# Performance work log

Measured on AMD Instinct MI355X. Metric: run time of the kernel, lower is better.

Reference implementation:

```python
import jax, jax.numpy as jnp
import numpy as np

ANNEAL_T_START = 5.0
T_END = 1.0


def setup_inputs() -> dict:
    key = jax.random.key(0)
    ks = jax.random.split(key, 8)
    B, V, H, CD, WID = 8192, 1024, 128, 16, 64
    return {
        "cond": jax.random.normal(ks[0], (B, CD), jnp.float32),
        "W": 0.01 * jax.random.normal(ks[1], (V, H), jnp.float32),
        "b": 0.01 * jax.random.normal(ks[2], (V,), jnp.float32),
        "c": 0.01 * jax.random.normal(ks[3], (H,), jnp.float32),
        "fc1_w": jax.random.normal(ks[4], (WID, CD), jnp.float32) / np.float32(np.sqrt(CD)),
        "fc1_b": jnp.zeros((WID,), jnp.float32),
        "fc2_w": jax.random.normal(ks[5], (2 * (V + H), WID), jnp.float32) / np.float32(np.sqrt(WID)),
        "fc2_b": jnp.zeros((2 * (V + H),), jnp.float32),
        "falloff": jnp.float32(1.0),
        "steps": 16,
    }


def _bern(key, p):
    # Bernoulli sample as float of same dtype as p.
    return (jax.random.uniform(key, p.shape, p.dtype) < p).astype(p.dtype)


def reference(cond, W, b, c, fc1_w, fc1_b, fc2_w, fc2_b, falloff, steps):
    V, H = W.shape
    B = cond.shape[0]
    dtype = W.dtype

    # Conditioner: FiLM-style modulation of visible/hidden biases.
    x = jnp.tanh(cond @ fc1_w.T + fc1_b)
    x = x @ fc2_w.T + fc2_b  # [B, 2*(V+H)]
    gamma_b = x[:, :V]
    beta_b = x[:, V:2 * V]
    gamma_c = x[:, 2 * V:2 * V + H]
    beta_c = x[:, 2 * V + H:]
    b_mod = (1.0 + gamma_b) * b + beta_b  # [B, V]
    c_mod = (1.0 + gamma_c) * c + beta_c  # [B, H]
    bsum = jnp.sum(b_mod, axis=-1)  # [B], constant across steps

    # Annealing temperature schedule (sigmoid falloff).
    t = jnp.arange(steps, dtype=dtype)
    s = 1.0 / (1.0 + jnp.exp(falloff * (t - steps / 2.0)))
    temps = T_END + (ANNEAL_T_START - T_END) * s  # [steps]

    base = jax.random.key(42)
    v0 = _bern(jax.random.fold_in(base, 2 ** 20), jnp.full((B, V), 0.5, dtype))
    s0_0 = jnp.ones((B, 1), dtype)

    def flip(v, s0):
        return s0 * v + (1.0 - s0) * (1.0 - v)

    def step(carry, xs):
        v, s0 = carry
        i, T = xs
        k1, k2, k3 = jax.random.split(jax.random.fold_in(base, i), 3)
        v_eff = flip(v, s0)
        p_h = jax.nn.sigmoid((v_eff @ W + c_mod) / T)  # [B, H]
        h = _bern(k1, p_h)
        a = h @ W.T  # [B, V]
        vb = jnp.sum(v * b_mod, axis=-1)
        va = jnp.sum(v * a, axis=-1)
        dE = -bsum - jnp.sum(a, axis=-1) + 2.0 * vb + 2.0 * va  # [B]
        p_s0 = jax.nn.sigmoid(dE / T)
        s0n = _bern(k2, p_s0)[:, None]  # [B, 1]
        p_v = jax.nn.sigmoid((a + b_mod) / T)
        v_samp = _bern(k3, p_v)
        v_next = flip(v_samp, s0n)
        return (v_next, s0n), None

    (v, _), _ = jax.lax.scan(
        step, (v0, s0_0), (jnp.arange(steps, dtype=jnp.int32), temps)
    )
    return v
```

## Files before the change

kernel.cpp:

```cpp
#include <hip/hip_runtime.h>
#include <stdint.h>

#pragma clang fp contract(off)

#define B_ 8192
#define V_ 1024
#define H_ 128
#define CD_ 16
#define WID_ 64
#define NOUT_ 2304
#define STEPS_ 16

typedef float f32x2 __attribute__((ext_vector_type(2)));

__device__ __forceinline__ void pkfma(f32x2& acc, f32x2 wv, f32x2 bf2) {
  asm("v_pk_fma_f32 %0, %1, %2, %0" : "+v"(acc) : "v"(wv), "v"(bf2));
}

__host__ __device__ __forceinline__ void tf2x32(uint32_t k0, uint32_t k1,
                                                uint32_t x0, uint32_t x1,
                                                uint32_t* o0, uint32_t* o1) {
  uint32_t ks2 = k0 ^ k1 ^ 0x1BD11BDAu;
#define RL_(v, d) (((v) << (d)) | ((v) >> (32 - (d))))
#define RND_(a) { x0 += x1; x1 = RL_(x1, a); x1 ^= x0; }
  x0 += k0; x1 += k1;
  RND_(13) RND_(15) RND_(26) RND_(6)
  x0 += k1; x1 += ks2 + 1u;
  RND_(17) RND_(29) RND_(16) RND_(24)
  x0 += ks2; x1 += k0 + 2u;
  RND_(13) RND_(15) RND_(26) RND_(6)
  x0 += k0; x1 += k1 + 3u;
  RND_(17) RND_(29) RND_(16) RND_(24)
  x0 += k1; x1 += ks2 + 4u;
  RND_(13) RND_(15) RND_(26) RND_(6)
  x0 += ks2; x1 += k0 + 5u;
#undef RND_
#undef RL_
  *o0 = x0; *o1 = x1;
}

struct Keys { uint32_t a[6]; };

__device__ __forceinline__ uint32_t draw_bits(uint32_t ka, uint32_t kb, uint32_t j) {
  uint32_t x0, x1;
  tf2x32(ka, kb, 0u, j, &x0, &x1);
  return x0 ^ x1;
}

__device__ __forceinline__ float bits_to_u(uint32_t bits) {
  return __fsub_rn(__uint_as_float((bits >> 9) | 0x3f800000u), 1.0f);
}

__device__ __forceinline__ float exp_a(float x) {
  float xc = fminf(fmaxf(x, -88.3762626647949f), 88.3762626647950f);
  float fx = floorf(__fadd_rn(__fmul_rn(xc, 1.44269504088896341f), 0.5f));
  float xr = __fsub_rn(xc, __fmul_rn(0.693359375f, fx));
  xr = __fsub_rn(xr, __fmul_rn(-2.12194440e-4f, fx));
  float zz = __fmul_rn(xr, xr);
  float y = 1.9875691500E-4f;
  y = __fadd_rn(__fmul_rn(y, xr), 1.3981999507E-3f);
  y = __fadd_rn(__fmul_rn(y, xr), 8.3334519073E-3f);
  y = __fadd_rn(__fmul_rn(y, xr), 4.1665795894E-2f);
  y = __fadd_rn(__fmul_rn(y, xr), 1.6666665459E-1f);
  y = __fadd_rn(__fmul_rn(y, xr), 5.0000001201E-1f);
  y = __fadd_rn(__fmul_rn(y, zz), xr);
  y = __fadd_rn(y, 1.0f);
  int n = (int)fx;
  float sc = __int_as_float((n + 127) << 23);
  return __fmul_rn(y, sc);
}

__device__ __forceinline__ float tanh_a(float xin) {
  float x = fmaxf(fminf(xin, 7.90531110763549805f), -7.90531110763549805f);
  float x2 = __fmul_rn(x, x);
  float p = __fadd_rn(__fmul_rn(x2, -2.76076847742355e-16f), 2.00018790482477e-13f);
  p = __fadd_rn(__fmul_rn(x2, p), -8.60467152213735e-11f);
  p = __fadd_rn(__fmul_rn(x2, p), 5.12229709037114e-08f);
  p = __fadd_rn(__fmul_rn(x2, p), 1.48572235717979e-05f);
  p = __fadd_rn(__fmul_rn(x2, p), 6.37261928875436e-04f);
  p = __fadd_rn(__fmul_rn(x2, p), 4.89352455891786e-03f);
  p = __fmul_rn(x, p);
  float q = __fadd_rn(__fmul_rn(x2, 1.19825839466702e-06f), 1.18534705686654e-04f);
  q = __fadd_rn(__fmul_rn(x2, q), 2.26843463243900e-03f);
  q = __fadd_rn(__fmul_rn(x2, q), 4.89352518554385e-03f);
  float r = p / q;
  if (fabsf(xin) < 0.0004f) r = xin;
  return r;
}

__device__ __forceinline__ float sigmoid_a(float z) {
  float e = exp_a(-z);
  return 1.0f / __fadd_rn(1.0f, e);
}

__global__ void k_transpose(const float* __restrict__ W, float* __restrict__ WT,
                            const float* __restrict__ fc2w, float* __restrict__ fc2T) {
  int i = blockIdx.x * blockDim.x + threadIdx.x;
  if (i < V_ * H_) { int v = i / H_, h = i % H_; WT[h * V_ + v] = W[i]; }
  if (i < NOUT_ * WID_) { int j = i / WID_, w = i % WID_; fc2T[w * NOUT_ + j] = fc2w[i]; }
}

__global__ void k_temps(const float* __restrict__ falloff, float* __restrict__ temps) {
  int t = threadIdx.x;
  if (t < 16) {
    float arg = __fmul_rn(*falloff, __fsub_rn((float)t, 8.0f));
    float e = exp_a(arg);
    float s = 1.0f / __fadd_rn(1.0f, e);
    temps[t] = __fadd_rn(1.0f, __fmul_rn(4.0f, s));
  }
}

__global__ void k_mlp1(const float* __restrict__ cond, const float* __restrict__ fc1w,
                       const float* __restrict__ fc1b, float* __restrict__ xout) {
  int idx = blockIdx.x * blockDim.x + threadIdx.x;
  if (idx >= B_ * WID_) return;
  int row = idx >> 6, w = idx & 63;
  float acc = 0.0f;
  for (int k = 0; k < CD_; k++) acc = __fmaf_rn(cond[row * CD_ + k], fc1w[w * CD_ + k], acc);
  float z = __fadd_rn(acc, fc1b[w]);
  xout[idx] = tanh_a(z);
}

__global__ __launch_bounds__(128) void k_mlp2b(const float* __restrict__ xmlp,
                       const float* __restrict__ fc2T, const float* __restrict__ fc2b,
                       const float* __restrict__ bvec, float* __restrict__ b_mod) {
  __shared__ float xs[32][WID_];
  int jbase = blockIdx.x * 128;
  int r0 = blockIdx.y * 32;
  int tid = threadIdx.x;
  for (int t = tid; t < 32 * WID_; t += 128)
    xs[t >> 6][t & 63] = xmlp[(r0 + (t >> 6)) * WID_ + (t & 63)];
  __syncthreads();
  int j = jbase + tid;
  float accg[32], accb[32];
#pragma unroll
  for (int r = 0; r < 32; r++) { accg[r] = 0.0f; accb[r] = 0.0f; }
  for (int w = 0; w < WID_; w++) {
    float fg = fc2T[w * NOUT_ + j];
    float fb = fc2T[w * NOUT_ + 1024 + j];
#pragma unroll
    for (int r = 0; r < 32; r++) {
      float xv = xs[r][w];
      accg[r] = __fmaf_rn(xv, fg, accg[r]);
      accb[r] = __fmaf_rn(xv, fb, accb[r]);
    }
  }
  float bj = bvec[j];
  float biasg = fc2b[j], biasb = fc2b[1024 + j];
#pragma unroll
  for (int r = 0; r < 32; r++) {
    float g = __fadd_rn(accg[r], biasg);
    float bb = __fadd_rn(accb[r], biasb);
    float t1 = __fadd_rn(1.0f, g);
    b_mod[(r0 + r) * V_ + j] = __fadd_rn(__fmul_rn(t1, bj), bb);
  }
}

__global__ __launch_bounds__(128) void k_mlp2c(const float* __restrict__ xmlp,
                       const float* __restrict__ fc2T, const float* __restrict__ fc2b,
                       const float* __restrict__ cvec, float* __restrict__ c_mod) {
  __shared__ float xs[32][WID_];
  int r0 = blockIdx.y * 32;
  int tid = threadIdx.x;
  for (int t = tid; t < 32 * WID_; t += 128)
    xs[t >> 6][t & 63] = xmlp[(r0 + (t >> 6)) * WID_ + (t & 63)];
  __syncthreads();
  float accg[32], accb[32];
#pragma unroll
  for (int r = 0; r < 32; r++) { accg[r] = 0.0f; accb[r] = 0.0f; }
  for (int w = 0; w < WID_; w++) {
    float fg = fc2T[w * NOUT_ + 2048 + tid];
    float fb = fc2T[w * NOUT_ + 2176 + tid];
#pragma unroll
    for (int r = 0; r < 32; r++) {
      float xv = xs[r][w];
      accg[r] = __fmaf_rn(xv, fg, accg[r]);
      accb[r] = __fmaf_rn(xv, fb, accb[r]);
    }
  }
  float cj = cvec[tid];
  float biasg = fc2b[2048 + tid], biasb = fc2b[2176 + tid];
#pragma unroll
  for (int r = 0; r < 32; r++) {
    float g = __fadd_rn(accg[r], biasg);
    float bb = __fadd_rn(accb[r], biasb);
    float t1 = __fadd_rn(1.0f, g);
    c_mod[(r0 + r) * H_ + tid] = __fadd_rn(__fmul_rn(t1, cj), bb);
  }
}

__global__ __launch_bounds__(64) void k_bsum(const float* __restrict__ b_mod,
                                             float* __restrict__ bsum) {
  int row = blockIdx.x * 64 + threadIdx.x;
  const float4* bp = (const float4*)(b_mod + (size_t)row * V_);
  float acc = 0.0f;
  for (int c = 0; c < 32; c++) {
    float4 Bv[8];
#pragma unroll
    for (int q = 0; q < 8; q++) Bv[q] = bp[c * 8 + q];
#pragma unroll
    for (int q = 0; q < 8; q++) {
      acc = __fadd_rn(acc, Bv[q].x);
      acc = __fadd_rn(acc, Bv[q].y);
      acc = __fadd_rn(acc, Bv[q].z);
      acc = __fadd_rn(acc, Bv[q].w);
    }
  }
  bsum[row] = acc;
}

__global__ void k_v0(uint32_t* __restrict__ v_bits, float* __restrict__ s0,
                     uint32_t kva, uint32_t kvb) {
  int idx = blockIdx.x * blockDim.x + threadIdx.x;
  int row = idx >> 10, col = idx & 1023;
  uint32_t bits = draw_bits(kva, kvb, (uint32_t)idx);
  float u = bits_to_u(bits);
  unsigned long long m = __ballot(u < 0.5f);
  if ((threadIdx.x & 63) == 0) {
    v_bits[row * 32 + (col >> 5)] = (uint32_t)m;
    v_bits[row * 32 + (col >> 5) + 1] = (uint32_t)(m >> 32);
  }
  if (col == 0) s0[row] = 1.0f;
}

__global__ __launch_bounds__(256) void k_h(const float* __restrict__ W,
                   const float* __restrict__ c_mod, const uint32_t* __restrict__ v_bits,
                   uint32_t* __restrict__ h_bits, const float* __restrict__ temps,
                   int step, Keys kn) {
  __shared__ uint32_t nib[16][32];
  int tid = threadIdx.x;
  int ct = tid & 31;
  int rt = tid >> 5;
  int h0 = ct << 2;
  int row0 = blockIdx.x * 16 + rt * 2;
  float T = temps[step];
  f32x2 a00 = {0.f, 0.f}, a01 = {0.f, 0.f};
  f32x2 a10 = {0.f, 0.f}, a11 = {0.f, 0.f};
  const float* wp = W + h0;
  const uint4* vb0q = (const uint4*)(v_bits + (size_t)row0 * 32);
  const uint4* vb1q = (const uint4*)(v_bits + (size_t)(row0 + 1) * 32);

  float4 A[8], Bq[8];
  uint32_t m0, m1;
  auto LOADW = [&](float4* d, int kbase) {
#pragma unroll
    for (int i = 0; i < 8; i++)
      d[i] = *(const float4*)(wp + (size_t)(kbase + i) * H_);
  };
  auto DO8 = [&](const float4* wv) {
#pragma unroll
    for (int j = 0; j < 8; j++) {
      uint32_t s0m = (uint32_t)((int32_t)m0 >> 31); m0 <<= 1;
      uint32_t s1m = (uint32_t)((int32_t)m1 >> 31); m1 <<= 1;
      float bf0 = __uint_as_float(s0m & 0x3f800000u);
      float bf1 = __uint_as_float(s1m & 0x3f800000u);
      f32x2 wlo = {wv[j].x, wv[j].y};
      f32x2 whi = {wv[j].z, wv[j].w};
      f32x2 b0 = {bf0, bf0};
      f32x2 b1 = {bf1, bf1};
      pkfma(a00, wlo, b0); pkfma(a01, whi, b0);
      pkfma(a10, wlo, b1); pkfma(a11, whi, b1);
    }
  };

  uint4 q0 = vb0q[0], q1 = vb1q[0];
  uint4 q0n, q1n;
  LOADW(A, 0);
  for (int kq = 0; kq < 8; kq++) {
    if (kq < 7) { q0n = vb0q[kq + 1]; q1n = vb1q[kq + 1]; }
    const uint32_t w0s[4] = {q0.x, q0.y, q0.z, q0.w};
    const uint32_t w1s[4] = {q1.x, q1.y, q1.z, q1.w};
#pragma unroll
    for (int wq = 0; wq < 4; wq++) {
      int kb = kq * 128 + wq * 32;
      m0 = __brev(w0s[wq]);
      m1 = __brev(w1s[wq]);
      LOADW(Bq, kb + 8);  DO8(A);
      LOADW(A, kb + 16);  DO8(Bq);
      LOADW(Bq, kb + 24); DO8(A);
      if (kb + 32 < 1024) LOADW(A, kb + 32);
      DO8(Bq);
    }
    q0 = q0n; q1 = q1n;
  }

  const f32x2* accs[2][2] = {{&a00, &a01}, {&a10, &a11}};
#pragma unroll
  for (int r = 0; r < 2; r++) {
    int row = row0 + r;
    float4 cm = *(const float4*)(c_mod + (size_t)row * H_ + h0);
    const float cma[4] = {cm.x, cm.y, cm.z, cm.w};
    const float ac[4] = {(*accs[r][0])[0], (*accs[r][0])[1],
                         (*accs[r][1])[0], (*accs[r][1])[1]};
    uint32_t nb = 0;
#pragma unroll
    for (int e = 0; e < 4; e++) {
      float z = __fadd_rn(ac[e], cma[e]) / T;
      float p = sigmoid_a(z);
      uint32_t b = draw_bits(kn.a[0], kn.a[1], (uint32_t)(row * H_ + h0 + e));
      if (bits_to_u(b) < p) nb |= 1u << e;
    }
    nib[rt * 2 + r][ct] = nb;
  }
  __syncthreads();
  if (tid < 64) {
    int rloc = tid >> 2, wq = tid & 3;
    uint32_t word = 0;
#pragma unroll
    for (int i = 0; i < 8; i++) word |= nib[rloc][wq * 8 + i] << (4 * i);
    h_bits[(size_t)(blockIdx.x * 16 + rloc) * 4 + wq] = word;
  }
}

__global__ __launch_bounds__(256) void k_a(const float* __restrict__ WT,
                   const uint32_t* __restrict__ h_bits, const float* __restrict__ b_mod,
                   float* __restrict__ a, uint32_t* __restrict__ vb_new,
                   const float* __restrict__ temps, int step, Keys kn) {
  __shared__ uint32_t nib[32][65];
  int tid = threadIdx.x;
  int ct = tid & 63;
  int rt = tid >> 6;
  int v0 = blockIdx.x * 256 + (ct << 2);
  int r0 = blockIdx.y * 32 + rt * 8;
  f32x2 acc[8][2];
#pragma unroll
  for (int r = 0; r < 8; r++) { acc[r][0] = f32x2{0.f, 0.f}; acc[r][1] = f32x2{0.f, 0.f}; }
  uint4 hw[8];
#pragma unroll
  for (int r = 0; r < 8; r++) hw[r] = *(const uint4*)(h_bits + (size_t)(r0 + r) * 4);
  const float* wp0 = WT + v0;

  uint32_t m[8];
  float4 buf0[4], buf1[4];
  auto LOADG = [&](float4* d, int g) {
    const float* wp = wp0 + (size_t)(g * 4) * V_;
#pragma unroll
    for (int jj = 0; jj < 4; jj++) d[jj] = *(const float4*)(wp + (size_t)jj * V_);
  };
  auto COMP = [&](const float4* d) {
#pragma unroll
    for (int jj = 0; jj < 4; jj++) {
      f32x2 wlo = {d[jj].x, d[jj].y};
      f32x2 whi = {d[jj].z, d[jj].w};
#pragma unroll
      for (int r = 0; r < 8; r++) {
        uint32_t sm = (uint32_t)((int32_t)m[r] >> 31);
        m[r] <<= 1;
        float bf = __uint_as_float(sm & 0x3f800000u);
        f32x2 b2 = {bf, bf};
        pkfma(acc[r][0], wlo, b2);
        pkfma(acc[r][1], whi, b2);
      }
    }
  };

  LOADG(buf0, 0);
#pragma unroll
  for (int g = 0; g < 32; g++) {
    if ((g & 7) == 0) {
      const int s = g >> 3;
#pragma unroll
      for (int r = 0; r < 8; r++)
        m[r] = __brev(s == 0 ? hw[r].x : s == 1 ? hw[r].y : s == 2 ? hw[r].z : hw[r].w);
    }
    if (g & 1) { if (g < 31) LOADG(buf0, g + 1); COMP(buf1); }
    else       { if (g < 31) LOADG(buf1, g + 1); COMP(buf0); }
  }

  float T = temps[step];
#pragma unroll
  for (int r = 0; r < 8; r++) {
    int row = r0 + r;
    float4 av = make_float4(acc[r][0][0], acc[r][0][1], acc[r][1][0], acc[r][1][1]);
    *(float4*)(a + (size_t)row * V_ + v0) = av;
    float4 bv = *(const float4*)(b_mod + (size_t)row * V_ + v0);
    const float ax[4] = {av.x, av.y, av.z, av.w};
    const float bx[4] = {bv.x, bv.y, bv.z, bv.w};
    uint32_t nb = 0;
#pragma unroll
    for (int e = 0; e < 4; e++) {
      float z = __fadd_rn(ax[e], bx[e]) / T;
      float p = sigmoid_a(z);
      uint32_t bits = draw_bits(kn.a[4], kn.a[5], (uint32_t)(row * V_ + v0 + e));
      float u = bits_to_u(bits);
      if (u < p) nb |= 1u << e;
    }
    nib[rt * 8 + r][ct] = nb;
  }
  __syncthreads();
  {
    int rloc = tid >> 3, wq = tid & 7;
    uint32_t word = 0;
#pragma unroll
    for (int i = 0; i < 8; i++) word |= nib[rloc][wq * 8 + i] << (4 * i);
    vb_new[(size_t)(blockIdx.y * 32 + rloc) * 32 + blockIdx.x * 8 + wq] = word;
  }
}

__global__ __launch_bounds__(256) void k_s0(const float* __restrict__ a,
                     const float* __restrict__ b_mod, const float* __restrict__ bsum,
                     const uint32_t* __restrict__ vb_old, float* __restrict__ s0,
                     const float* __restrict__ temps, int step, Keys kn) {
  __shared__ float As[2][16][132];
  __shared__ float Bs[2][16][132];
  int tid = threadIdx.x;
  int r0 = blockIdx.x * 16;

  auto STAGE = [&](int buf, int c) {
#pragma unroll
    for (int i = 0; i < 2; i++) {
      int e = tid + i * 256;
      int r = e >> 5, c4 = e & 31;
      float4 av = *(const float4*)(a + (size_t)(r0 + r) * V_ + c * 128 + c4 * 4);
      float4 bv = *(const float4*)(b_mod + (size_t)(r0 + r) * V_ + c * 128 + c4 * 4);
      *(float4*)&As[buf][r][c4 * 4] = av;
      *(float4*)&Bs[buf][r][c4 * 4] = bv;
    }
  };

  float suma = 0.0f, vb = 0.0f, va = 0.0f;
  uint32_t flipm = 0;
  if (tid < 16) flipm = (s0[r0 + tid] == 0.0f) ? 0xFFFFFFFFu : 0u;
  STAGE(0, 0);
  __syncthreads();
  for (int c = 0; c < 8; c++) {
    if (c < 7) STAGE((c + 1) & 1, c + 1);
    if (tid < 16) {
      int row = r0 + tid;
      uint4 mw = *(const uint4*)(vb_old + (size_t)row * 32 + c * 4);
      const uint32_t mm[4] = {mw.x ^ flipm, mw.y ^ flipm, mw.z ^ flipm, mw.w ^ flipm};
#pragma unroll
      for (int w4 = 0; w4 < 4; w4++) {
        uint32_t m = mm[w4];
#pragma unroll
        for (int j4 = 0; j4 < 8; j4++) {
          float4 av4 = *(const float4*)&As[c & 1][tid][w4 * 32 + j4 * 4];
          float4 bv4 = *(const float4*)&Bs[c & 1][tid][w4 * 32 + j4 * 4];
          const float ax[4] = {av4.x, av4.y, av4.z, av4.w};
          const float bx[4] = {bv4.x, bv4.y, bv4.z, bv4.w};
#pragma unroll
          for (int e = 0; e < 4; e++) {
            float bit = (float)((m >> (j4 * 4 + e)) & 1u);
            suma = __fadd_rn(suma, ax[e]);
            vb = __fmaf_rn(bx[e], bit, vb);
            va = __fmaf_rn(ax[e], bit, va);
          }
        }
      }
    }
    __syncthreads();
  }
  if (tid < 16) {
    int row = r0 + tid;
    float dE = __fsub_rn(-bsum[row], suma);
    dE = __fadd_rn(dE, __fmul_rn(2.0f, vb));
    dE = __fadd_rn(dE, __fmul_rn(2.0f, va));
    float T = temps[step];
    float p = sigmoid_a(dE / T);
    uint32_t bits = draw_bits(kn.a[2], kn.a[3], (uint32_t)row);
    float u = bits_to_u(bits);
    s0[row] = (u < p) ? 1.0f : 0.0f;
  }
}

__global__ void k_fin(const uint32_t* __restrict__ v_bits, const float* __restrict__ s0,
                      float* __restrict__ vout) {
  int idx = blockIdx.x * blockDim.x + threadIdx.x;
  int row = idx >> 10, col = idx & 1023;
  uint32_t w = v_bits[row * 32 + (col >> 5)];
  uint32_t bit = (w >> (col & 31)) & 1u;
  uint32_t eff = (s0[row] != 0.0f) ? bit : (bit ^ 1u);
  vout[idx] = (float)eff;
}

extern "C" void kernel_launch(void* const* d_in, const int* in_sizes, int n_in,
                              void* d_out, int out_size, void* d_ws, size_t ws_size,
                              hipStream_t stream) {
  const float* cond = (const float*)d_in[0];
  const float* W = (const float*)d_in[1];
  const float* bvec = (const float*)d_in[2];
  const float* cvec = (const float*)d_in[3];
  const float* fc1w = (const float*)d_in[4];
  const float* fc1b = (const float*)d_in[5];
  const float* fc2w = (const float*)d_in[6];
  const float* fc2b = (const float*)d_in[7];
  const float* falloff = (const float*)d_in[8];
  float* out = (float*)d_out;

  char* ws = (char*)d_ws;
  size_t off = 0;
  auto alloc = [&](size_t bytes) { void* p = ws + off; off += (bytes + 255) & ~(size_t)255; return p; };
  float* b_mod = (float*)alloc((size_t)B_ * V_ * 4);
  float* c_mod = (float*)alloc((size_t)B_ * H_ * 4);
  float* abuf  = (float*)alloc((size_t)B_ * V_ * 4);
  float* xmlp  = (float*)alloc((size_t)B_ * WID_ * 4);
  float* bsum  = (float*)alloc((size_t)B_ * 4);
  float* s0    = (float*)alloc((size_t)B_ * 4);
  uint32_t* v_bits0 = (uint32_t*)alloc((size_t)B_ * 32 * 4);
  uint32_t* v_bits1 = (uint32_t*)alloc((size_t)B_ * 32 * 4);
  uint32_t* h_bits = (uint32_t*)alloc((size_t)B_ * 4 * 4);
  float* WT    = (float*)alloc((size_t)H_ * V_ * 4);
  float* fc2T  = (float*)alloc((size_t)WID_ * NOUT_ * 4);
  float* temps = (float*)alloc(16 * 4);
  uint32_t* vb[2] = {v_bits0, v_bits1};

  uint32_t kva, kvb;
  tf2x32(0u, 42u, 0u, 1048576u, &kva, &kvb);
  Keys kn[16];
  for (int i = 0; i < 16; i++) {
    uint32_t f0, f1;
    tf2x32(0u, 42u, 0u, (uint32_t)i, &f0, &f1);
    uint32_t a0, a1;
    tf2x32(f0, f1, 0u, 0u, &a0, &a1); kn[i].a[0] = a0; kn[i].a[1] = a1;
    tf2x32(f0, f1, 0u, 1u, &a0, &a1); kn[i].a[2] = a0; kn[i].a[3] = a1;
    tf2x32(f0, f1, 0u, 2u, &a0, &a1); kn[i].a[4] = a0; kn[i].a[5] = a1;
  }

  k_transpose<<<(NOUT_ * WID_ + 255) / 256, 256, 0, stream>>>(W, WT, fc2w, fc2T);
  k_temps<<<1, 64, 0, stream>>>(falloff, temps);
  k_mlp1<<<(B_ * WID_) / 256, 256, 0, stream>>>(cond, fc1w, fc1b, xmlp);
  k_mlp2b<<<dim3(8, 256), 128, 0, stream>>>(xmlp, fc2T, fc2b, bvec, b_mod);
  k_mlp2c<<<dim3(1, 256), 128, 0, stream>>>(xmlp, fc2T, fc2b, cvec, c_mod);
  k_bsum<<<B_ / 64, 64, 0, stream>>>(b_mod, bsum);
  k_v0<<<(B_ * V_) / 256, 256, 0, stream>>>(vb[0], s0, kva, kvb);

  for (int i = 0; i < STEPS_; i++) {
    k_h<<<B_ / 16, 256, 0, stream>>>(W, c_mod, vb[i & 1], h_bits, temps, i, kn[i]);
    k_a<<<dim3(4, B_ / 32), 256, 0, stream>>>(WT, h_bits, b_mod, abuf,
                                              vb[(i + 1) & 1], temps, i, kn[i]);
    k_s0<<<B_ / 16, 256, 0, stream>>>(abuf, b_mod, bsum, vb[i & 1], s0, temps, i, kn[i]);
  }

  k_fin<<<(B_ * V_) / 256, 256, 0, stream>>>(vb[0], s0, out);
}
```

Baseline: 2.870 ms.

## Fuse visible-sampling and s0 energy kernels, keep activations in LDS

Merges k_a and k_s0 into one kernel, k_av. Each block covers 8 full rows, stages `a` and `b_mod` in shared memory, samples the new visible bits and computes the dE reduction and the s0 sample in the same pass. This removes the global `a` buffer and its write and re-read every step, and drops one launch per step. k_h now computes one row per thread group instead of two, which halves reuse of each W load per row. The fused kernel uses about 66 KB of LDS per block, which limits occupancy, and it keeps the serial 8-thread reduction tail.

```diff
diff --git a/kernel.cpp b/kernel.cpp
--- a/kernel.cpp
+++ b/kernel.cpp
@@ -227,21 +227,19 @@
                    const float* __restrict__ c_mod, const uint32_t* __restrict__ v_bits,
                    uint32_t* __restrict__ h_bits, const float* __restrict__ temps,
                    int step, Keys kn) {
-  __shared__ uint32_t nib[16][32];
+  __shared__ uint32_t nib[8][32];
   int tid = threadIdx.x;
   int ct = tid & 31;
   int rt = tid >> 5;
   int h0 = ct << 2;
-  int row0 = blockIdx.x * 16 + rt * 2;
+  int row = blockIdx.x * 8 + rt;
   float T = temps[step];
-  f32x2 a00 = {0.f, 0.f}, a01 = {0.f, 0.f};
-  f32x2 a10 = {0.f, 0.f}, a11 = {0.f, 0.f};
+  f32x2 a0 = {0.f, 0.f}, a1 = {0.f, 0.f};
   const float* wp = W + h0;
-  const uint4* vb0q = (const uint4*)(v_bits + (size_t)row0 * 32);
-  const uint4* vb1q = (const uint4*)(v_bits + (size_t)(row0 + 1) * 32);
+  const uint4* vbq = (const uint4*)(v_bits + (size_t)row * 32);
 
   float4 A[8], Bq[8];
-  uint32_t m0, m1;
+  uint32_t m0;
   auto LOADW = [&](float4* d, int kbase) {
 #pragma unroll
     for (int i = 0; i < 8; i++)
@@ -251,47 +249,37 @@
 #pragma unroll
     for (int j = 0; j < 8; j++) {
       uint32_t s0m = (uint32_t)((int32_t)m0 >> 31); m0 <<= 1;
-      uint32_t s1m = (uint32_t)((int32_t)m1 >> 31); m1 <<= 1;
       float bf0 = __uint_as_float(s0m & 0x3f800000u);
-      float bf1 = __uint_as_float(s1m & 0x3f800000u);
       f32x2 wlo = {wv[j].x, wv[j].y};
       f32x2 whi = {wv[j].z, wv[j].w};
       f32x2 b0 = {bf0, bf0};
-      f32x2 b1 = {bf1, bf1};
-      pkfma(a00, wlo, b0); pkfma(a01, whi, b0);
-      pkfma(a10, wlo, b1); pkfma(a11, whi, b1);
+      pkfma(a0, wlo, b0); pkfma(a1, whi, b0);
     }
   };
 
-  uint4 q0 = vb0q[0], q1 = vb1q[0];
-  uint4 q0n, q1n;
+  uint4 q0 = vbq[0];
+  uint4 q0n;
   LOADW(A, 0);
   for (int kq = 0; kq < 8; kq++) {
-    if (kq < 7) { q0n = vb0q[kq + 1]; q1n = vb1q[kq + 1]; }
+    if (kq < 7) q0n = vbq[kq + 1];
     const uint32_t w0s[4] = {q0.x, q0.y, q0.z, q0.w};
-    const uint32_t w1s[4] = {q1.x, q1.y, q1.z, q1.w};
 #pragma unroll
     for (int wq = 0; wq < 4; wq++) {
       int kb = kq * 128 + wq * 32;
       m0 = __brev(w0s[wq]);
-      m1 = __brev(w1s[wq]);
       LOADW(Bq, kb + 8);  DO8(A);
       LOADW(A, kb + 16);  DO8(Bq);
       LOADW(Bq, kb + 24); DO8(A);
       if (kb + 32 < 1024) LOADW(A, kb + 32);
       DO8(Bq);
     }
-    q0 = q0n; q1 = q1n;
-  }
-
-  const f32x2* accs[2][2] = {{&a00, &a01}, {&a10, &a11}};
-#pragma unroll
-  for (int r = 0; r < 2; r++) {
-    int row = row0 + r;
+    q0 = q0n;
+  }
+
+  {
     float4 cm = *(const float4*)(c_mod + (size_t)row * H_ + h0);
     const float cma[4] = {cm.x, cm.y, cm.z, cm.w};
-    const float ac[4] = {(*accs[r][0])[0], (*accs[r][0])[1],
-                         (*accs[r][1])[0], (*accs[r][1])[1]};
+    const float ac[4] = {a0[0], a0[1], a1[0], a1[1]};
     uint32_t nb = 0;
 #pragma unroll
     for (int e = 0; e < 4; e++) {
@@ -300,28 +288,30 @@
       uint32_t b = draw_bits(kn.a[0], kn.a[1], (uint32_t)(row * H_ + h0 + e));
       if (bits_to_u(b) < p) nb |= 1u << e;
     }
-    nib[rt * 2 + r][ct] = nb;
+    nib[rt][ct] = nb;
   }
   __syncthreads();
-  if (tid < 64) {
+  if (tid < 32) {
     int rloc = tid >> 2, wq = tid & 3;
     uint32_t word = 0;
 #pragma unroll
     for (int i = 0; i < 8; i++) word |= nib[rloc][wq * 8 + i] << (4 * i);
-    h_bits[(size_t)(blockIdx.x * 16 + rloc) * 4 + wq] = word;
-  }
-}
-
-__global__ __launch_bounds__(256) void k_a(const float* __restrict__ WT,
+    h_bits[(size_t)(blockIdx.x * 8 + rloc) * 4 + wq] = word;
+  }
+}
+
+__global__ __launch_bounds__(256) void k_av(const float* __restrict__ WT,
                    const uint32_t* __restrict__ h_bits, const float* __restrict__ b_mod,
-                   float* __restrict__ a, uint32_t* __restrict__ vb_new,
-                   const float* __restrict__ temps, int step, Keys kn) {
-  __shared__ uint32_t nib[32][65];
+                   const float* __restrict__ bsum,
+                   const uint32_t* __restrict__ vb_old, uint32_t* __restrict__ vb_new,
+                   float* __restrict__ s0, const float* __restrict__ temps,
+                   int step, Keys kn) {
+  __shared__ float As[8][1028];
+  __shared__ float Bs[8][1028];
+  __shared__ uint32_t nib[8][256];
   int tid = threadIdx.x;
-  int ct = tid & 63;
-  int rt = tid >> 6;
-  int v0 = blockIdx.x * 256 + (ct << 2);
-  int r0 = blockIdx.y * 32 + rt * 8;
+  int v0 = tid << 2;
+  int r0 = blockIdx.x * 8;
   f32x2 acc[8][2];
 #pragma unroll
   for (int r = 0; r < 8; r++) { acc[r][0] = f32x2{0.f, 0.f}; acc[r][1] = f32x2{0.f, 0.f}; }
@@ -368,12 +358,15 @@
   }
 
   float T = temps[step];
+  uint32_t flipm = 0;
+  if (tid < 8) flipm = (s0[r0 + tid] == 0.0f) ? 0xFFFFFFFFu : 0u;
 #pragma unroll
   for (int r = 0; r < 8; r++) {
     int row = r0 + r;
     float4 av = make_float4(acc[r][0][0], acc[r][0][1], acc[r][1][0], acc[r][1][1]);
-    *(float4*)(a + (size_t)row * V_ + v0) = av;
+    *(float4*)&As[r][v0] = av;
     float4 bv = *(const float4*)(b_mod + (size_t)row * V_ + v0);
+    *(float4*)&Bs[r][v0] = bv;
     const float ax[4] = {av.x, av.y, av.z, av.w};
     const float bx[4] = {bv.x, bv.y, bv.z, bv.w};
     uint32_t nb = 0;
@@ -385,62 +378,34 @@
       float u = bits_to_u(bits);
       if (u < p) nb |= 1u << e;
     }
-    nib[rt * 8 + r][ct] = nb;
+    nib[r][tid] = nb;
   }
   __syncthreads();
   {
-    int rloc = tid >> 3, wq = tid & 7;
+    int rloc = tid >> 5, wq = tid & 31;
     uint32_t word = 0;
 #pragma unroll
     for (int i = 0; i < 8; i++) word |= nib[rloc][wq * 8 + i] << (4 * i);
-    vb_new[(size_t)(blockIdx.y * 32 + rloc) * 32 + blockIdx.x * 8 + wq] = word;
-  }
-}
-
-__global__ __launch_bounds__(256) void k_s0(const float* __restrict__ a,
-                     const float* __restrict__ b_mod, const float* __restrict__ bsum,
-                     const uint32_t* __restrict__ vb_old, float* __restrict__ s0,
-                     const float* __restrict__ temps, int step, Keys kn) {
-  __shared__ float As[2][16][132];
-  __shared__ float Bs[2][16][132];
-  int tid = threadIdx.x;
-  int r0 = blockIdx.x * 16;
-
-  auto STAGE = [&](int buf, int c) {
-#pragma unroll
-    for (int i = 0; i < 2; i++) {
-      int e = tid + i * 256;
-      int r = e >> 5, c4 = e & 31;
-      float4 av = *(const float4*)(a + (size_t)(r0 + r) * V_ + c * 128 + c4 * 4);
-      float4 bv = *(const float4*)(b_mod + (size_t)(r0 + r) * V_ + c * 128 + c4 * 4);
-      *(float4*)&As[buf][r][c4 * 4] = av;
-      *(float4*)&Bs[buf][r][c4 * 4] = bv;
-    }
-  };
-
-  float suma = 0.0f, vb = 0.0f, va = 0.0f;
-  uint32_t flipm = 0;
-  if (tid < 16) flipm = (s0[r0 + tid] == 0.0f) ? 0xFFFFFFFFu : 0u;
-  STAGE(0, 0);
-  __syncthreads();
-  for (int c = 0; c < 8; c++) {
-    if (c < 7) STAGE((c + 1) & 1, c + 1);
-    if (tid < 16) {
-      int row = r0 + tid;
+    vb_new[(size_t)(r0 + rloc) * 32 + wq] = word;
+  }
+  if (tid < 8) {
+    int row = r0 + tid;
+    float suma = 0.0f, vb = 0.0f, va = 0.0f;
+    for (int c = 0; c < 8; c++) {
       uint4 mw = *(const uint4*)(vb_old + (size_t)row * 32 + c * 4);
       const uint32_t mm[4] = {mw.x ^ flipm, mw.y ^ flipm, mw.z ^ flipm, mw.w ^ flipm};
 #pragma unroll
       for (int w4 = 0; w4 < 4; w4++) {
-        uint32_t m = mm[w4];
+        uint32_t mloc = mm[w4];
 #pragma unroll
         for (int j4 = 0; j4 < 8; j4++) {
-          float4 av4 = *(const float4*)&As[c & 1][tid][w4 * 32 + j4 * 4];
-          float4 bv4 = *(const float4*)&Bs[c & 1][tid][w4 * 32 + j4 * 4];
+          float4 av4 = *(const float4*)&As[tid][c * 128 + w4 * 32 + j4 * 4];
+          float4 bv4 = *(const float4*)&Bs[tid][c * 128 + w4 * 32 + j4 * 4];
           const float ax[4] = {av4.x, av4.y, av4.z, av4.w};
           const float bx[4] = {bv4.x, bv4.y, bv4.z, bv4.w};
 #pragma unroll
           for (int e = 0; e < 4; e++) {
-            float bit = (float)((m >> (j4 * 4 + e)) & 1u);
+            float bit = (float)((mloc >> (j4 * 4 + e)) & 1u);
             suma = __fadd_rn(suma, ax[e]);
             vb = __fmaf_rn(bx[e], bit, vb);
             va = __fmaf_rn(ax[e], bit, va);
@@ -448,14 +413,9 @@
         }
       }
     }
-    __syncthreads();
-  }
-  if (tid < 16) {
-    int row = r0 + tid;
     float dE = __fsub_rn(-bsum[row], suma);
     dE = __fadd_rn(dE, __fmul_rn(2.0f, vb));
     dE = __fadd_rn(dE, __fmul_rn(2.0f, va));
-    float T = temps[step];
     float p = sigmoid_a(dE / T);
     uint32_t bits = draw_bits(kn.a[2], kn.a[3], (uint32_t)row);
     float u = bits_to_u(bits);
@@ -492,7 +452,6 @@
   auto alloc = [&](size_t bytes) { void* p = ws + off; off += (bytes + 255) & ~(size_t)255; return p; };
   float* b_mod = (float*)alloc((size_t)B_ * V_ * 4);
   float* c_mod = (float*)alloc((size_t)B_ * H_ * 4);
-  float* abuf  = (float*)alloc((size_t)B_ * V_ * 4);
   float* xmlp  = (float*)alloc((size_t)B_ * WID_ * 4);
   float* bsum  = (float*)alloc((size_t)B_ * 4);
   float* s0    = (float*)alloc((size_t)B_ * 4);
@@ -525,10 +484,9 @@
   k_v0<<<(B_ * V_) / 256, 256, 0, stream>>>(vb[0], s0, kva, kvb);
 
   for (int i = 0; i < STEPS_; i++) {
-    k_h<<<B_ / 16, 256, 0, stream>>>(W, c_mod, vb[i & 1], h_bits, temps, i, kn[i]);
-    k_a<<<dim3(4, B_ / 32), 256, 0, stream>>>(WT, h_bits, b_mod, abuf,
-                                              vb[(i + 1) & 1], temps, i, kn[i]);
-    k_s0<<<B_ / 16, 256, 0, stream>>>(abuf, b_mod, bsum, vb[i & 1], s0, temps, i, kn[i]);
+    k_h<<<B_ / 8, 256, 0, stream>>>(W, c_mod, vb[i & 1], h_bits, temps, i, kn[i]);
+    k_av<<<B_ / 8, 256, 0, stream>>>(WT, h_bits, b_mod, bsum, vb[i & 1],
+                                     vb[(i + 1) & 1], s0, temps, i, kn[i]);
   }
 
   k_fin<<<(B_ * V_) / 256, 256, 0, stream>>>(vb[0], s0, out);
```

Result: slower. 4.901 ms (+70.8%).
